# Optimization experiments

Measured on AMD Instinct MI355X. Metric: run time of the kernel, lower is better.

Reference implementation:

```python
import jax, jax.numpy as jnp
import numpy as np

B, C, Q, E = 32, 1024, 128, 512

def setup_inputs() -> dict:
    key = jax.random.key(0)
    k1, k2, k3 = jax.random.split(key, 3)
    context = jax.random.normal(k1, (B, C, E), dtype=jnp.float32)
    question = jax.random.normal(k2, (B, Q, E), dtype=jnp.float32)
    # ws = [ws_q | ws_c | ws_m], matching cat([q, ctx, q*ctx]) order
    ws = jax.random.normal(k3, (3 * E,), dtype=jnp.float32) * (1.0 / np.sqrt(E))
    return {"context": context, "question": question, "ws": ws}

def reference(context, question, ws):
    ws_q, ws_c, ws_m = ws[:E], ws[E:2 * E], ws[2 * E:]
    # similarity[b,c,q] = ws_q.q[b,q] + ws_c.c[b,c] + ws_m.(q[b,q]*c[b,c])
    sim = (jnp.einsum('bqe,e->bq', question, ws_q)[:, None, :]
           + jnp.einsum('bce,e->bc', context, ws_c)[:, :, None]
           + jnp.einsum('bce,bqe,e->bcq', context, question, ws_m))  # (B,C,Q)
    c2q = jnp.einsum('bcq,bqe->bce', jax.nn.softmax(sim, axis=2), question)  # (B,C,E)
    q2c_w = jax.nn.softmax(jnp.max(sim, axis=2), axis=1)  # (B,C)
    q2c = jnp.einsum('bc,bce->be', q2c_w, context)[:, None, :]  # (B,1,E)
    return (c2q, q2c)
```

## Files before the change

kernel.cpp:

```cpp
#include <hip/hip_runtime.h>

#define BB 32
#define CC 1024
#define QQ 128
#define EE 512

typedef unsigned int uint32;
typedef unsigned short u16;
typedef __bf16 bf16x8 __attribute__((ext_vector_type(8)));
typedef float f32x4 __attribute__((ext_vector_type(4)));

#define QMF_OFF  (0u)
#define QTF_OFF  (4u<<20)
#define PV_OFF   (8u<<20)
#define QDP_OFF  (12u<<20)
#define MT_OFF   ((12u<<20) + 65536u)
#define ST_OFF   (MT_OFF + 8192u)

__device__ __forceinline__ u16 bfc(float f){
  __bf16 h = (__bf16)f;
  return __builtin_bit_cast(u16, h);
}
__device__ __forceinline__ float bf2f(uint32 lo16){
  return __builtin_bit_cast(float, lo16 << 16);
}

__global__ __launch_bounds__(256) void k_prep(const float* __restrict__ q,
                                              const float* __restrict__ ws,
                                              unsigned char* __restrict__ wsp){
  const int b = blockIdx.x >> 2, et = blockIdx.x & 3, e0 = et*128;
  __shared__ u16 tm[128*136];
  __shared__ u16 tt[128*136];
  const int tid = threadIdx.x;
  float* qdp = (float*)(wsp + QDP_OFF) + (size_t)(b*4 + et)*128;
  #pragma unroll
  for (int i=0;i<16;i++){
    int id = tid + i*256;
    int qi = id >> 5;
    int el = (id & 31) << 2;
    float4 v = *(const float4*)(q + (size_t)(b*QQ+qi)*EE + e0 + el);
    float4 a = *(const float4*)(ws +          e0 + el);
    float4 c = *(const float4*)(ws +   EE +   e0 + el);
    float4 m = *(const float4*)(ws + 2*EE +   e0 + el);
    ushort4 um; um.x = bfc(v.x*m.x + c.x); um.y = bfc(v.y*m.y + c.y);
                um.z = bfc(v.z*m.z + c.z); um.w = bfc(v.w*m.w + c.w);
    *(ushort4*)&tm[qi*136 + el] = um;
    ushort4 ut; ut.x = bfc(v.x); ut.y = bfc(v.y); ut.z = bfc(v.z); ut.w = bfc(v.w);
    *(ushort4*)&tt[qi*136 + el] = ut;
    float d = v.x*a.x + v.y*a.y + v.z*a.z + v.w*a.w;
    d += __shfl_xor(d,1); d += __shfl_xor(d,2); d += __shfl_xor(d,4);
    d += __shfl_xor(d,8); d += __shfl_xor(d,16);
    if ((tid & 31) == 0) qdp[qi] = d;
  }
  __syncthreads();
  const int lane = tid & 63, wv = tid >> 6, l15 = lane & 15, l4 = lane >> 4;
  uint4* qmf = (uint4*)(wsp + QMF_OFF);
  uint4* qtf = (uint4*)(wsp + QTF_OFF);
  #pragma unroll
  for (int i=0;i<8;i++){
    int f = wv*8 + i;
    int kl = f >> 3, nf = f & 7;
    uint4 u = *(const uint4*)&tm[(nf*16 + l15)*136 + kl*32 + l4*8];
    qmf[(size_t)((b*16 + et*4 + kl)*8 + nf)*64 + lane] = u;
  }
  #pragma unroll
  for (int i=0;i<8;i++){
    int f = wv*8 + i;
    int ks2 = f >> 3, nl = f & 7, ne = et*8 + nl;
    uint32 x[4];
    #pragma unroll
    for (int p=0;p<4;p++){
      u16 t0 = tt[(ks2*32 + l4*8 + 2*p    )*136 + nl*16 + l15];
      u16 t1 = tt[(ks2*32 + l4*8 + 2*p + 1)*136 + nl*16 + l15];
      x[p] = (uint32)t0 | ((uint32)t1 << 16);
    }
    uint4 u; u.x = x[0]; u.y = x[1]; u.z = x[2]; u.w = x[3];
    qtf[(size_t)((b*4 + ks2)*32 + ne)*64 + lane] = u;
  }
}

__global__ __attribute__((amdgpu_flat_work_group_size(512, 512)))
           __attribute__((amdgpu_waves_per_eu(2)))
void k_main(const float* __restrict__ ctx,
            unsigned char* __restrict__ wsp,
            float* __restrict__ out){
  __shared__ __align__(16) unsigned char buf[2][65536];
  __shared__ __align__(16) float mxA[2][64*8];
  __shared__ __align__(16) float smA[2][64*8];
  __shared__ float wrowA[2][4][16];

  const int bid = blockIdx.x;
  const int sw  = (bid & 7)*32 + (bid >> 3);
  const int b   = sw >> 3;
  const int pr  = sw & 7;
  const int t0  = pr*2, t1 = pr*2 + 1;
  const int tid = threadIdx.x;
  const int lane = tid & 63;
  const int w    = tid >> 6;
  const int l15  = lane & 15;
  const int l4   = lane >> 4;
  const int rg   = w >> 1;
  const int eh   = w & 1;

  const float4* cb0 = (const float4*)(ctx + (size_t)(b*CC + t0*64)*EE);
  const float4* cb1 = (const float4*)(ctx + (size_t)(b*CC + t1*64)*EE);
  float4 v[16];
  #pragma unroll
  for (int i=0;i<16;i++) v[i] = cb0[i*512 + tid];

  const uint4* qmf4 = (const uint4*)(wsp + QMF_OFF);
  bf16x8 a[16];
  #pragma unroll
  for (int ks=0; ks<16; ks++)
    a[ks] = __builtin_bit_cast(bf16x8, qmf4[(size_t)((b*16 + ks)*8 + w)*64 + lane]);
  float qdv[4];
  {
    const float* qdp = (const float*)(wsp + QDP_OFF) + (size_t)b*512;
    #pragma unroll
    for (int r=0;r<4;r++){
      const int qi = w*16 + l4*4 + r;
      qdv[r] = qdp[qi] + qdp[128+qi] + qdp[256+qi] + qdp[384+qi];
    }
  }

  const int colb = (tid & 127)*8;
  auto stage_write = [&](unsigned char* dst){
    #pragma unroll
    for (int i=0;i<16;i++){
      int row = i*4 + (tid >> 7);
      uint2 u;
      u.x = (uint32)bfc(v[i].x) | ((uint32)bfc(v[i].y) << 16);
      u.y = (uint32)bfc(v[i].z) | ((uint32)bfc(v[i].w) << 16);
      *(uint2*)(dst + row*1024 + (colb ^ ((row & 7) << 4))) = u;
    }
  };

  stage_write(buf[0]);
  __syncthreads();

  #pragma unroll
  for (int i=0;i<16;i++) v[i] = cb1[i*512 + tid];

  auto gemm1 = [&](const unsigned char* bp, f32x4* acc){
    #pragma unroll
    for (int cc=0;cc<4;cc++) acc[cc] = (f32x4){0.f,0.f,0.f,0.f};
    #pragma unroll
    for (int ks=0; ks<16; ks++){
      #pragma unroll
      for (int cc=0; cc<4; cc++){
        const int row = cc*16 + l15;
        bf16x8 bf = __builtin_bit_cast(bf16x8,
          *(const uint4*)(bp + row*1024 + ((ks*64 + l4*16) ^ ((row & 7) << 4))));
        acc[cc] = __builtin_amdgcn_mfma_f32_16x16x32_bf16(a[ks], bf, acc[cc], 0, 0, 0);
      }
    }
  };
  f32x4 acc[4];
  gemm1(buf[0], acc);
  __syncthreads();

  auto softmax = [&](int ti, f32x4* ac){
    #pragma unroll
    for (int cc=0; cc<4; cc++){
      float m = -3.0e38f, s = 0.f;
      u16 hb[4];
      #pragma unroll
      for (int r=0;r<4;r++){
        float vv = ac[cc][r] + qdv[r];
        vv = fminf(vv, 80.f);
        m = fmaxf(m, vv);
        u16 h = bfc(__expf(vv));
        hb[r] = h;
        s += bf2f(h);
      }
      uint2 u; u.x = (uint32)hb[0] | ((uint32)hb[1]<<16);
               u.y = (uint32)hb[2] | ((uint32)hb[3]<<16);
      *(uint2*)(buf[ti] + (cc*4 + (w>>1))*1024 + (((w&1)*2 + (l4>>1))*16 + l15)*16 + (l4&1)*8) = u;
      m = fmaxf(m, __shfl_xor(m, 16)); m = fmaxf(m, __shfl_xor(m, 32));
      s += __shfl_xor(s, 16);          s += __shfl_xor(s, 32);
      if (l4 == 0){
        mxA[ti][(cc*16 + l15)*8 + w] = m;
        smA[ti][(cc*16 + l15)*8 + w] = s;
      }
    }
  };
  softmax(0, acc);
  stage_write(buf[1]);
  __syncthreads();

  auto rden_of = [&](int ti, float* rd){
    #pragma unroll
    for (int r=0;r<4;r++){
      const int c = rg*16 + l4*4 + r;
      f32x4 s0 = *(const f32x4*)&smA[ti][c*8];
      f32x4 s1 = *(const f32x4*)&smA[ti][c*8 + 4];
      rd[r] = 1.f/(s0[0]+s0[1]+s0[2]+s0[3]+s1[0]+s1[1]+s1[2]+s1[3]);
    }
  };
  auto q2c_stats = [&](int ti, int tglob){
    if (eh != 0) return;
    float mf[4];
    #pragma unroll
    for (int r=0;r<4;r++){
      const int c = rg*16 + l4*4 + r;
      f32x4 m0 = *(const f32x4*)&mxA[ti][c*8];
      f32x4 m1 = *(const f32x4*)&mxA[ti][c*8 + 4];
      mf[r] = fmaxf(fmaxf(fmaxf(m0[0],m0[1]), fmaxf(m0[2],m0[3])),
                    fmaxf(fmaxf(m1[0],m1[1]), fmaxf(m1[2],m1[3])));
    }
    float m16 = fmaxf(fmaxf(mf[0],mf[1]), fmaxf(mf[2],mf[3]));
    m16 = fmaxf(m16, __shfl_xor(m16, 16));
    m16 = fmaxf(m16, __shfl_xor(m16, 32));
    float wr[4], s16 = 0.f;
    #pragma unroll
    for (int r=0;r<4;r++){ wr[r] = __expf(mf[r] - m16); s16 += wr[r]; }
    s16 += __shfl_xor(s16, 16);
    s16 += __shfl_xor(s16, 32);
    if (l15 == 0){
      #pragma unroll
      for (int r=0;r<4;r++) wrowA[ti][rg][l4*4 + r] = wr[r];
    }
    if (lane == 0){
      ((float*)(wsp + MT_OFF))[b*64 + tglob*4 + rg] = m16;
      ((float*)(wsp + ST_OFF))[b*64 + tglob*4 + rg] = s16;
    }
  };

  float rden0[4], rden1[4];
  rden_of(0, rden0);
  q2c_stats(0, t0);
  bf16x8 pa0[4], pa1[4];
  #pragma unroll
  for (int k2=0;k2<4;k2++)
    pa0[k2] = __builtin_bit_cast(bf16x8, *(const uint4*)(buf[0] + (rg*4 + k2)*1024 + lane*16));

  unsigned char* qstage = buf[0] + 16384;
  const unsigned char* qtfb = wsp + QTF_OFF + (size_t)b*131072;
  auto dma = [&](int p){
    #pragma unroll
    for (int j=0;j<2;j++){
      const int f = w*2 + j;
      const int ks2 = f >> 2, nl = f & 3;
      const unsigned char* g = qtfb + (size_t)(ks2*32 + p*4 + nl)*1024 + lane*16;
      __builtin_amdgcn_global_load_lds(
        (const __attribute__((address_space(1))) uint32*)g,
        (__attribute__((address_space(3))) uint32*)(qstage + (p&1)*16384 + f*1024),
        16, 0, 0);
    }
  };
  dma(0);

  gemm1(buf[1], acc);
  __syncthreads();
  softmax(1, acc);
  __syncthreads();
  rden_of(1, rden1);
  q2c_stats(1, t1);
  #pragma unroll
  for (int k2=0;k2<4;k2++)
    pa1[k2] = __builtin_bit_cast(bf16x8, *(const uint4*)(buf[1] + (rg*4 + k2)*1024 + lane*16));

  float* ob0 = out + (size_t)(b*CC + t0*64 + rg*16)*EE;
  float* ob1 = out + (size_t)(b*CC + t1*64 + rg*16)*EE;
  #pragma unroll
  for (int p=0; p<8; p++){
    if (p < 7) dma(p+1);
    const unsigned char* qs = qstage + (p&1)*16384;
    f32x4 A0 = (f32x4){0.f,0.f,0.f,0.f};
    f32x4 A1 = (f32x4){0.f,0.f,0.f,0.f};
    f32x4 B0 = (f32x4){0.f,0.f,0.f,0.f};
    f32x4 B1 = (f32x4){0.f,0.f,0.f,0.f};
    #pragma unroll
    for (int k2=0;k2<4;k2++){
      bf16x8 b0 = __builtin_bit_cast(bf16x8, *(const uint4*)(qs + (k2*4 + eh*2 + 0)*1024 + lane*16));
      bf16x8 b1 = __builtin_bit_cast(bf16x8, *(const uint4*)(qs + (k2*4 + eh*2 + 1)*1024 + lane*16));
      A0 = __builtin_amdgcn_mfma_f32_16x16x32_bf16(pa0[k2], b0, A0, 0, 0, 0);
      A1 = __builtin_amdgcn_mfma_f32_16x16x32_bf16(pa0[k2], b1, A1, 0, 0, 0);
      B0 = __builtin_amdgcn_mfma_f32_16x16x32_bf16(pa1[k2], b0, B0, 0, 0, 0);
      B1 = __builtin_amdgcn_mfma_f32_16x16x32_bf16(pa1[k2], b1, B1, 0, 0, 0);
    }
    #pragma unroll
    for (int r=0;r<4;r++){
      const size_t ro = (size_t)(l4*4 + r)*EE + p*64 + eh*32;
      ob0[ro +      l15] = A0[r]*rden0[r];
      ob0[ro + 16 + l15] = A1[r]*rden0[r];
      ob1[ro +      l15] = B0[r]*rden1[r];
      ob1[ro + 16 + l15] = B1[r]*rden1[r];
    }
    __syncthreads();
  }

  #pragma unroll
  for (int ti=0; ti<2; ti++){
    const int tg = ti ? t1 : t0;
    const float4* cq = (const float4*)(ctx + (size_t)(b*CC + tg*64 + rg*16)*EE + eh*256) + lane;
    float4 a4; a4.x = 0.f; a4.y = 0.f; a4.z = 0.f; a4.w = 0.f;
    #pragma unroll
    for (int rr=0; rr<16; rr++){
      float wv = wrowA[ti][rg][rr];
      float4 g = cq[(size_t)rr*128];
      a4.x = fmaf(wv, g.x, a4.x); a4.y = fmaf(wv, g.y, a4.y);
      a4.z = fmaf(wv, g.z, a4.z); a4.w = fmaf(wv, g.w, a4.w);
    }
    float* pv = (float*)(wsp + PV_OFF) + (size_t)(b*64 + tg*4 + rg)*EE + eh*256 + lane*4;
    *(float4*)pv = a4;
  }
}

__global__ __launch_bounds__(256) void k_fin(unsigned char* __restrict__ wsp,
                                             float* __restrict__ out){
  const int b = blockIdx.x;
  __shared__ float sc_s[64];
  const int tid = threadIdx.x;
  if (tid < 64){
    float Mg = ((const float*)(wsp + MT_OFF))[b*64 + tid];
    float Sg = ((const float*)(wsp + ST_OFF))[b*64 + tid];
    float M = Mg;
    #pragma unroll
    for (int off=1; off<64; off<<=1) M = fmaxf(M, __shfl_xor(M, off));
    float ev = __expf(Mg - M);
    float ds = ev * Sg;
    #pragma unroll
    for (int off=1; off<64; off<<=1) ds += __shfl_xor(ds, off);
    sc_s[tid] = ev / ds;
  }
  __syncthreads();
  const float* pv = (const float*)(wsp + PV_OFF) + (size_t)b*64*EE;
  float a0 = 0.f, a1 = 0.f;
  #pragma unroll 8
  for (int g=0; g<64; g++){
    float s = sc_s[g];
    a0 = fmaf(s, pv[g*EE + tid],       a0);
    a1 = fmaf(s, pv[g*EE + tid + 256], a1);
  }
  size_t base = (size_t)BB*CC*EE + (size_t)b*EE;
  out[base + tid]       = a0;
  out[base + tid + 256] = a1;
}

extern "C" void kernel_launch(void* const* d_in, const int* in_sizes, int n_in,
                              void* d_out, int out_size, void* d_ws, size_t ws_size,
                              hipStream_t stream){
  const float* ctx = (const float*)d_in[0];
  const float* q   = (const float*)d_in[1];
  const float* ws  = (const float*)d_in[2];
  float* out = (float*)d_out;
  unsigned char* wsp = (unsigned char*)d_ws;

  k_prep<<<dim3(BB*4), dim3(256), 0, stream>>>(q, ws, wsp);
  k_main<<<dim3(256),  dim3(512), 0, stream>>>(ctx, wsp, out);
  k_fin <<<dim3(BB),   dim3(256), 0, stream>>>(wsp, out);
}
```

Measured before the change: 59.22 us.

## Stream 16-row context tiles per block with resident question in LDS and online q2c

Each block now owns a 128-row context segment and loops over 16-row tiles. Every tile prefetches the next context chunk, runs both GEMMs and stores its c2q rows. The whole transposed question for the batch is loaded into LDS once up front, which replaces the per-phase DMA ring. q2c is built with an online softmax over the tiles, using the bf16 context already staged in LDS rather than re-reading context from global memory. This cuts k_fin's reduction from 64 partials to 8. The cost is a very large LDS footprint (about 150KB, which limits occupancy), four barriers per tile, and small serial tiles that may leave MFMA latency exposed. q2c also now uses bf16-rounded context values.

Result: slower. 108.2 us (+82.8%).

```diff
diff --git a/kernel.cpp b/kernel.cpp
--- a/kernel.cpp
+++ b/kernel.cpp
@@ -12,10 +12,12 @@
 
 #define QMF_OFF  (0u)
 #define QTF_OFF  (4u<<20)
-#define PV_OFF   (8u<<20)
-#define QDP_OFF  (12u<<20)
-#define MT_OFF   ((12u<<20) + 65536u)
-#define ST_OFF   (MT_OFF + 8192u)
+#define QDP_OFF  (8u<<20)
+#define PVB_OFF  ((8u<<20) + 65536u)
+#define MB_OFF   (PVB_OFF + 524288u)
+#define SB_OFF   (MB_OFF + 1024u)
+
+#define RAWBAR() asm volatile("s_waitcnt lgkmcnt(0)\n\ts_barrier" ::: "memory")
 
 __device__ __forceinline__ u16 bfc(float f){
   __bf16 h = (__bf16)f;
@@ -84,34 +86,45 @@
 void k_main(const float* __restrict__ ctx,
             unsigned char* __restrict__ wsp,
             float* __restrict__ out){
-  __shared__ __align__(16) unsigned char buf[2][65536];
-  __shared__ __align__(16) float mxA[2][64*8];
-  __shared__ __align__(16) float smA[2][64*8];
-  __shared__ float wrowA[2][4][16];
+  __shared__ __align__(16) unsigned char qlds[131072];
+  __shared__ __align__(16) unsigned char buf[16384];
+  __shared__ __align__(16) unsigned char pfrag[4096];
+  __shared__ float mx_s[16*8];
+  __shared__ float sm_s[16*8];
+  __shared__ float wrow_s[16];
+  __shared__ float scale_s;
+  __shared__ float Mblk_s, Sblk_s;
 
   const int bid = blockIdx.x;
   const int sw  = (bid & 7)*32 + (bid >> 3);
   const int b   = sw >> 3;
-  const int pr  = sw & 7;
-  const int t0  = pr*2, t1 = pr*2 + 1;
+  const int seg = sw & 7;
   const int tid = threadIdx.x;
   const int lane = tid & 63;
   const int w    = tid >> 6;
   const int l15  = lane & 15;
   const int l4   = lane >> 4;
-  const int rg   = w >> 1;
-  const int eh   = w & 1;
-
-  const float4* cb0 = (const float4*)(ctx + (size_t)(b*CC + t0*64)*EE);
-  const float4* cb1 = (const float4*)(ctx + (size_t)(b*CC + t1*64)*EE);
-  float4 v[16];
-  #pragma unroll
-  for (int i=0;i<16;i++) v[i] = cb0[i*512 + tid];
+
+  if (tid == 0){ Mblk_s = -3.0e38f; Sblk_s = 0.f; }
+
+  const unsigned char* qtfb = wsp + QTF_OFF + (size_t)b*131072;
+  #pragma unroll
+  for (int j=0;j<16;j++){
+    const int f = w*16 + j;
+    __builtin_amdgcn_global_load_lds(
+      (const __attribute__((address_space(1))) uint32*)(qtfb + (size_t)f*1024 + lane*16),
+      (__attribute__((address_space(3))) uint32*)(qlds + f*1024), 16, 0, 0);
+  }
+
+  const float4* cseg = (const float4*)(ctx + (size_t)(b*CC + seg*128)*EE);
+  float4 v[4];
+  #pragma unroll
+  for (int k=0;k<4;k++) v[k] = cseg[k*512 + tid];
 
   const uint4* qmf4 = (const uint4*)(wsp + QMF_OFF);
   bf16x8 a[16];
   #pragma unroll
-  for (int ks=0; ks<16; ks++)
+  for (int ks=0;ks<16;ks++)
     a[ks] = __builtin_bit_cast(bf16x8, qmf4[(size_t)((b*16 + ks)*8 + w)*64 + lane]);
   float qdv[4];
   {
@@ -123,51 +136,42 @@
     }
   }
 
-  const int colb = (tid & 127)*8;
-  auto stage_write = [&](unsigned char* dst){
-    #pragma unroll
-    for (int i=0;i<16;i++){
-      int row = i*4 + (tid >> 7);
-      uint2 u;
-      u.x = (uint32)bfc(v[i].x) | ((uint32)bfc(v[i].y) << 16);
-      u.y = (uint32)bfc(v[i].z) | ((uint32)bfc(v[i].w) << 16);
-      *(uint2*)(dst + row*1024 + (colb ^ ((row & 7) << 4))) = u;
-    }
-  };
-
-  stage_write(buf[0]);
-  __syncthreads();
-
-  #pragma unroll
-  for (int i=0;i<16;i++) v[i] = cb1[i*512 + tid];
-
-  auto gemm1 = [&](const unsigned char* bp, f32x4* acc){
-    #pragma unroll
-    for (int cc=0;cc<4;cc++) acc[cc] = (f32x4){0.f,0.f,0.f,0.f};
+  float pv = 0.f;
+  float* ob_base = out + (size_t)(b*CC + seg*128)*EE;
+
+  #pragma unroll
+  for (int i=0;i<8;i++){
+    {
+      const int colb = (tid & 127)*8;
+      #pragma unroll
+      for (int k=0;k<4;k++){
+        const int row = k*4 + (tid >> 7);
+        uint2 u;
+        u.x = (uint32)bfc(v[k].x) | ((uint32)bfc(v[k].y) << 16);
+        u.y = (uint32)bfc(v[k].z) | ((uint32)bfc(v[k].w) << 16);
+        *(uint2*)(buf + row*1024 + (colb ^ ((row & 7) << 4))) = u;
+      }
+    }
+    if (i < 7){
+      #pragma unroll
+      for (int k=0;k<4;k++) v[k] = cseg[(i+1)*2048 + k*512 + tid];
+    }
+    RAWBAR();
+
+    f32x4 acc = (f32x4){0.f,0.f,0.f,0.f};
     #pragma unroll
     for (int ks=0; ks<16; ks++){
-      #pragma unroll
-      for (int cc=0; cc<4; cc++){
-        const int row = cc*16 + l15;
-        bf16x8 bf = __builtin_bit_cast(bf16x8,
-          *(const uint4*)(bp + row*1024 + ((ks*64 + l4*16) ^ ((row & 7) << 4))));
-        acc[cc] = __builtin_amdgcn_mfma_f32_16x16x32_bf16(a[ks], bf, acc[cc], 0, 0, 0);
-      }
-    }
-  };
-  f32x4 acc[4];
-  gemm1(buf[0], acc);
-  __syncthreads();
-
-  auto softmax = [&](int ti, f32x4* ac){
-    #pragma unroll
-    for (int cc=0; cc<4; cc++){
+      bf16x8 bf = __builtin_bit_cast(bf16x8,
+        *(const uint4*)(buf + l15*1024 + ((ks*64 + l4*16) ^ ((l15 & 7) << 4))));
+      acc = __builtin_amdgcn_mfma_f32_16x16x32_bf16(a[ks], bf, acc, 0, 0, 0);
+    }
+
+    {
       float m = -3.0e38f, s = 0.f;
       u16 hb[4];
       #pragma unroll
       for (int r=0;r<4;r++){
-        float vv = ac[cc][r] + qdv[r];
-        vv = fminf(vv, 80.f);
+        float vv = fminf(acc[r] + qdv[r], 80.f);
         m = fmaxf(m, vv);
         u16 h = bfc(__expf(vv));
         hb[r] = h;
@@ -175,167 +179,117 @@
       }
       uint2 u; u.x = (uint32)hb[0] | ((uint32)hb[1]<<16);
                u.y = (uint32)hb[2] | ((uint32)hb[3]<<16);
-      *(uint2*)(buf[ti] + (cc*4 + (w>>1))*1024 + (((w&1)*2 + (l4>>1))*16 + l15)*16 + (l4&1)*8) = u;
+      *(uint2*)(pfrag + (w>>1)*1024 + (((w&1)*2 + (l4>>1))*16 + l15)*16 + (l4&1)*8) = u;
       m = fmaxf(m, __shfl_xor(m, 16)); m = fmaxf(m, __shfl_xor(m, 32));
       s += __shfl_xor(s, 16);          s += __shfl_xor(s, 32);
-      if (l4 == 0){
-        mxA[ti][(cc*16 + l15)*8 + w] = m;
-        smA[ti][(cc*16 + l15)*8 + w] = s;
-      }
-    }
-  };
-  softmax(0, acc);
-  stage_write(buf[1]);
-  __syncthreads();
-
-  auto rden_of = [&](int ti, float* rd){
+      if (l4 == 0){ mx_s[l15*8 + w] = m; sm_s[l15*8 + w] = s; }
+    }
+    RAWBAR();
+
+    float rden[4];
     #pragma unroll
     for (int r=0;r<4;r++){
-      const int c = rg*16 + l4*4 + r;
-      f32x4 s0 = *(const f32x4*)&smA[ti][c*8];
-      f32x4 s1 = *(const f32x4*)&smA[ti][c*8 + 4];
-      rd[r] = 1.f/(s0[0]+s0[1]+s0[2]+s0[3]+s1[0]+s1[1]+s1[2]+s1[3]);
-    }
-  };
-  auto q2c_stats = [&](int ti, int tglob){
-    if (eh != 0) return;
-    float mf[4];
-    #pragma unroll
-    for (int r=0;r<4;r++){
-      const int c = rg*16 + l4*4 + r;
-      f32x4 m0 = *(const f32x4*)&mxA[ti][c*8];
-      f32x4 m1 = *(const f32x4*)&mxA[ti][c*8 + 4];
-      mf[r] = fmaxf(fmaxf(fmaxf(m0[0],m0[1]), fmaxf(m0[2],m0[3])),
-                    fmaxf(fmaxf(m1[0],m1[1]), fmaxf(m1[2],m1[3])));
-    }
-    float m16 = fmaxf(fmaxf(mf[0],mf[1]), fmaxf(mf[2],mf[3]));
-    m16 = fmaxf(m16, __shfl_xor(m16, 16));
-    m16 = fmaxf(m16, __shfl_xor(m16, 32));
-    float wr[4], s16 = 0.f;
-    #pragma unroll
-    for (int r=0;r<4;r++){ wr[r] = __expf(mf[r] - m16); s16 += wr[r]; }
-    s16 += __shfl_xor(s16, 16);
-    s16 += __shfl_xor(s16, 32);
-    if (l15 == 0){
-      #pragma unroll
-      for (int r=0;r<4;r++) wrowA[ti][rg][l4*4 + r] = wr[r];
-    }
-    if (lane == 0){
-      ((float*)(wsp + MT_OFF))[b*64 + tglob*4 + rg] = m16;
-      ((float*)(wsp + ST_OFF))[b*64 + tglob*4 + rg] = s16;
-    }
-  };
-
-  float rden0[4], rden1[4];
-  rden_of(0, rden0);
-  q2c_stats(0, t0);
-  bf16x8 pa0[4], pa1[4];
-  #pragma unroll
-  for (int k2=0;k2<4;k2++)
-    pa0[k2] = __builtin_bit_cast(bf16x8, *(const uint4*)(buf[0] + (rg*4 + k2)*1024 + lane*16));
-
-  unsigned char* qstage = buf[0] + 16384;
-  const unsigned char* qtfb = wsp + QTF_OFF + (size_t)b*131072;
-  auto dma = [&](int p){
-    #pragma unroll
-    for (int j=0;j<2;j++){
-      const int f = w*2 + j;
-      const int ks2 = f >> 2, nl = f & 3;
-      const unsigned char* g = qtfb + (size_t)(ks2*32 + p*4 + nl)*1024 + lane*16;
-      __builtin_amdgcn_global_load_lds(
-        (const __attribute__((address_space(1))) uint32*)g,
-        (__attribute__((address_space(3))) uint32*)(qstage + (p&1)*16384 + f*1024),
-        16, 0, 0);
-    }
-  };
-  dma(0);
-
-  gemm1(buf[1], acc);
-  __syncthreads();
-  softmax(1, acc);
-  __syncthreads();
-  rden_of(1, rden1);
-  q2c_stats(1, t1);
-  #pragma unroll
-  for (int k2=0;k2<4;k2++)
-    pa1[k2] = __builtin_bit_cast(bf16x8, *(const uint4*)(buf[1] + (rg*4 + k2)*1024 + lane*16));
-
-  float* ob0 = out + (size_t)(b*CC + t0*64 + rg*16)*EE;
-  float* ob1 = out + (size_t)(b*CC + t1*64 + rg*16)*EE;
-  #pragma unroll
-  for (int p=0; p<8; p++){
-    if (p < 7) dma(p+1);
-    const unsigned char* qs = qstage + (p&1)*16384;
-    f32x4 A0 = (f32x4){0.f,0.f,0.f,0.f};
-    f32x4 A1 = (f32x4){0.f,0.f,0.f,0.f};
-    f32x4 B0 = (f32x4){0.f,0.f,0.f,0.f};
-    f32x4 B1 = (f32x4){0.f,0.f,0.f,0.f};
+      const float* sp = &sm_s[(l4*4 + r)*8];
+      rden[r] = 1.f/(sp[0]+sp[1]+sp[2]+sp[3]+sp[4]+sp[5]+sp[6]+sp[7]);
+    }
+    bf16x8 pa[4];
+    #pragma unroll
+    for (int k2=0;k2<4;k2++)
+      pa[k2] = __builtin_bit_cast(bf16x8, *(const uint4*)(pfrag + k2*1024 + lane*16));
+
+    if (w == 0 && lane < 16){
+      const float* mp = &mx_s[lane*8];
+      float mf = fmaxf(fmaxf(fmaxf(mp[0],mp[1]),fmaxf(mp[2],mp[3])),
+                       fmaxf(fmaxf(mp[4],mp[5]),fmaxf(mp[6],mp[7])));
+      float tm = mf;
+      tm = fmaxf(tm, __shfl_xor(tm,1)); tm = fmaxf(tm, __shfl_xor(tm,2));
+      tm = fmaxf(tm, __shfl_xor(tm,4)); tm = fmaxf(tm, __shfl_xor(tm,8));
+      float Mold = Mblk_s;
+      float Mnew = fmaxf(Mold, tm);
+      float wr = __expf(mf - Mnew);
+      wrow_s[lane] = wr;
+      float ssum = wr;
+      ssum += __shfl_xor(ssum,1); ssum += __shfl_xor(ssum,2);
+      ssum += __shfl_xor(ssum,4); ssum += __shfl_xor(ssum,8);
+      if (lane == 0){
+        float sc = __expf(Mold - Mnew);
+        scale_s = sc;
+        Sblk_s  = Sblk_s*sc + ssum;
+        Mblk_s  = Mnew;
+      }
+    }
+
+    f32x4 acc2[4];
+    #pragma unroll
+    for (int n=0;n<4;n++) acc2[n] = (f32x4){0.f,0.f,0.f,0.f};
     #pragma unroll
     for (int k2=0;k2<4;k2++){
-      bf16x8 b0 = __builtin_bit_cast(bf16x8, *(const uint4*)(qs + (k2*4 + eh*2 + 0)*1024 + lane*16));
-      bf16x8 b1 = __builtin_bit_cast(bf16x8, *(const uint4*)(qs + (k2*4 + eh*2 + 1)*1024 + lane*16));
-      A0 = __builtin_amdgcn_mfma_f32_16x16x32_bf16(pa0[k2], b0, A0, 0, 0, 0);
-      A1 = __builtin_amdgcn_mfma_f32_16x16x32_bf16(pa0[k2], b1, A1, 0, 0, 0);
-      B0 = __builtin_amdgcn_mfma_f32_16x16x32_bf16(pa1[k2], b0, B0, 0, 0, 0);
-      B1 = __builtin_amdgcn_mfma_f32_16x16x32_bf16(pa1[k2], b1, B1, 0, 0, 0);
-    }
-    #pragma unroll
-    for (int r=0;r<4;r++){
-      const size_t ro = (size_t)(l4*4 + r)*EE + p*64 + eh*32;
-      ob0[ro +      l15] = A0[r]*rden0[r];
-      ob0[ro + 16 + l15] = A1[r]*rden0[r];
-      ob1[ro +      l15] = B0[r]*rden1[r];
-      ob1[ro + 16 + l15] = B1[r]*rden1[r];
-    }
-    __syncthreads();
-  }
-
-  #pragma unroll
-  for (int ti=0; ti<2; ti++){
-    const int tg = ti ? t1 : t0;
-    const float4* cq = (const float4*)(ctx + (size_t)(b*CC + tg*64 + rg*16)*EE + eh*256) + lane;
-    float4 a4; a4.x = 0.f; a4.y = 0.f; a4.z = 0.f; a4.w = 0.f;
-    #pragma unroll
-    for (int rr=0; rr<16; rr++){
-      float wv = wrowA[ti][rg][rr];
-      float4 g = cq[(size_t)rr*128];
-      a4.x = fmaf(wv, g.x, a4.x); a4.y = fmaf(wv, g.y, a4.y);
-      a4.z = fmaf(wv, g.z, a4.z); a4.w = fmaf(wv, g.w, a4.w);
-    }
-    float* pv = (float*)(wsp + PV_OFF) + (size_t)(b*64 + tg*4 + rg)*EE + eh*256 + lane*4;
-    *(float4*)pv = a4;
+      #pragma unroll
+      for (int n=0;n<4;n++){
+        bf16x8 bq = __builtin_bit_cast(bf16x8,
+          *(const uint4*)(qlds + (size_t)(k2*32 + w*4 + n)*1024 + lane*16));
+        acc2[n] = __builtin_amdgcn_mfma_f32_16x16x32_bf16(pa[k2], bq, acc2[n], 0, 0, 0);
+      }
+    }
+    float* ob = ob_base + (size_t)i*16*EE + w*64;
+    #pragma unroll
+    for (int n=0;n<4;n++){
+      #pragma unroll
+      for (int r=0;r<4;r++)
+        ob[(size_t)(l4*4 + r)*EE + n*16 + l15] = acc2[n][r]*rden[r];
+    }
+    RAWBAR();
+
+    {
+      const float sc = scale_s;
+      float add = 0.f;
+      #pragma unroll
+      for (int rr=0; rr<16; rr++){
+        uint32 x = *(const u16*)(buf + rr*1024 + ((tid*2) ^ ((rr & 7) << 4)));
+        add = fmaf(wrow_s[rr], bf2f(x), add);
+      }
+      pv = pv*sc + add;
+    }
+    RAWBAR();
+  }
+
+  ((float*)(wsp + PVB_OFF))[(size_t)(b*8 + seg)*512 + tid] = pv;
+  if (tid == 0){
+    ((float*)(wsp + MB_OFF))[b*8 + seg] = Mblk_s;
+    ((float*)(wsp + SB_OFF))[b*8 + seg] = Sblk_s;
   }
 }
 
 __global__ __launch_bounds__(256) void k_fin(unsigned char* __restrict__ wsp,
                                              float* __restrict__ out){
   const int b = blockIdx.x;
-  __shared__ float sc_s[64];
+  __shared__ float sc_s[8];
+  __shared__ float dinv_s;
   const int tid = threadIdx.x;
-  if (tid < 64){
-    float Mg = ((const float*)(wsp + MT_OFF))[b*64 + tid];
-    float Sg = ((const float*)(wsp + ST_OFF))[b*64 + tid];
-    float M = Mg;
-    #pragma unroll
-    for (int off=1; off<64; off<<=1) M = fmaxf(M, __shfl_xor(M, off));
-    float ev = __expf(Mg - M);
-    float ds = ev * Sg;
-    #pragma unroll
-    for (int off=1; off<64; off<<=1) ds += __shfl_xor(ds, off);
-    sc_s[tid] = ev / ds;
+  if (tid < 8){
+    float Mk = ((const float*)(wsp + MB_OFF))[b*8 + tid];
+    float Sk = ((const float*)(wsp + SB_OFF))[b*8 + tid];
+    float M = Mk;
+    M = fmaxf(M, __shfl_xor(M,1)); M = fmaxf(M, __shfl_xor(M,2)); M = fmaxf(M, __shfl_xor(M,4));
+    float ev = __expf(Mk - M);
+    float d = ev*Sk;
+    d += __shfl_xor(d,1); d += __shfl_xor(d,2); d += __shfl_xor(d,4);
+    sc_s[tid] = ev;
+    if (tid == 0) dinv_s = 1.f/d;
   }
   __syncthreads();
-  const float* pv = (const float*)(wsp + PV_OFF) + (size_t)b*64*EE;
+  const float* pvb = (const float*)(wsp + PVB_OFF) + (size_t)b*8*512;
   float a0 = 0.f, a1 = 0.f;
-  #pragma unroll 8
-  for (int g=0; g<64; g++){
-    float s = sc_s[g];
-    a0 = fmaf(s, pv[g*EE + tid],       a0);
-    a1 = fmaf(s, pv[g*EE + tid + 256], a1);
+  #pragma unroll
+  for (int k=0;k<8;k++){
+    float s = sc_s[k];
+    a0 = fmaf(s, pvb[k*512 + tid],       a0);
+    a1 = fmaf(s, pvb[k*512 + tid + 256], a1);
   }
   size_t base = (size_t)BB*CC*EE + (size_t)b*EE;
-  out[base + tid]       = a0;
-  out[base + tid + 256] = a1;
+  float di = dinv_s;
+  out[base + tid]       = a0*di;
+  out[base + tid + 256] = a1*di;
 }
 
 extern "C" void kernel_launch(void* const* d_in, const int* in_sizes, int n_in,
```
